# Optimization experiments

Hardware: AMD Instinct MI355X
Metric: run time of the kernel (lower is better)

The kernel has to match this reference:

```python
import jax, jax.numpy as jnp
import numpy as np

BS, SEQ, ML, DEPTH = 32, 50, 16, 4
NN = 2 ** DEPTH - 1          # 15 nodes per complete binary tree (heap layout)
VOCAB, EMB, ENC = 50000, 128, 128
GH = 32                      # bigru hidden per direction
NC = 100                     # num_concepts
LH = 128                     # LSTM hidden
LIN = 2 + 2 * GH + NC + 1    # 167 LSTM feature dim


def _gru_dir(x, Wx, Wh, bx, bh, reverse):
    # x: [B, T, I]; torch GRU gate order r,z,n
    B, H = x.shape[0], Wh.shape[1]
    xe = jnp.einsum('bti,gi->btg', x, Wx) + bx   # [B,T,3H]
    xs = jnp.swapaxes(xe, 0, 1)
    if reverse:
        xs = xs[::-1]
    def step(h, xt):
        gh = h @ Wh.T + bh
        r = jax.nn.sigmoid(xt[:, :H] + gh[:, :H])
        z = jax.nn.sigmoid(xt[:, H:2 * H] + gh[:, H:2 * H])
        n = jnp.tanh(xt[:, 2 * H:] + r * gh[:, 2 * H:])
        hn = (1.0 - z) * n + z * h
        return hn, hn
    _, hs = jax.lax.scan(step, jnp.zeros((B, H), x.dtype), xs)
    if reverse:
        hs = hs[::-1]
    return jnp.swapaxes(hs, 0, 1)


def _lstm(x, Wx, Wh, bx, bh):
    # x: [B, T, I]; torch LSTM gate order i,f,g,o
    B, H = x.shape[0], Wh.shape[1]
    xe = jnp.einsum('bti,gi->btg', x, Wx) + bx   # [B,T,4H]
    def step(carry, xt):
        h, c = carry
        g = xt + h @ Wh.T + bh
        i = jax.nn.sigmoid(g[:, :H])
        f = jax.nn.sigmoid(g[:, H:2 * H])
        gg = jnp.tanh(g[:, 2 * H:3 * H])
        o = jax.nn.sigmoid(g[:, 3 * H:])
        c = f * c + i * gg
        h = o * jnp.tanh(c)
        return (h, c), h
    h0 = (jnp.zeros((B, H), x.dtype), jnp.zeros((B, H), x.dtype))
    _, hs = jax.lax.scan(step, h0, jnp.swapaxes(xe, 0, 1))
    return jnp.swapaxes(hs, 0, 1)


def setup_inputs() -> dict:
    key = jax.random.key(0)
    ks = jax.random.split(key, 24)
    p = {}
    p['p_id'] = jax.random.randint(ks[0], (BS, SEQ), 0, 1000)
    p['c_id'] = jax.random.randint(ks[1], (BS, SEQ), 0, NC)
    p['ast_tokens'] = jax.random.randint(ks[2], (BS, SEQ, ML, NN), 0, VOCAB)
    p['target_c'] = jax.nn.one_hot(jax.random.randint(ks[3], (BS, SEQ), 0, NC + 1), NC + 1, dtype=jnp.float32)
    p['c_embed'] = jax.random.normal(ks[4], (BS, SEQ, NC + 1), jnp.float32)
    p['cur_result'] = jax.random.normal(ks[5], (BS, SEQ, 2), jnp.float32)
    p['result'] = (jax.random.uniform(ks[6], (BS * SEQ,)) < 0.5).astype(jnp.float32)
    p['emb'] = jax.random.normal(ks[7], (VOCAB, EMB), jnp.float32) * 0.02
    p['Wc_w'] = jax.random.normal(ks[8], (ENC, EMB), jnp.float32) / np.sqrt(EMB)
    p['Wc_b'] = jnp.zeros((ENC,), jnp.float32)
    p['gru_WxF'] = jax.random.normal(ks[9], (3 * GH, ENC), jnp.float32) / np.sqrt(ENC)
    p['gru_WhF'] = jax.random.normal(ks[10], (3 * GH, GH), jnp.float32) / np.sqrt(GH)
    p['gru_bxF'] = jnp.zeros((3 * GH,), jnp.float32)
    p['gru_bhF'] = jnp.zeros((3 * GH,), jnp.float32)
    p['gru_WxB'] = jax.random.normal(ks[11], (3 * GH, ENC), jnp.float32) / np.sqrt(ENC)
    p['gru_WhB'] = jax.random.normal(ks[12], (3 * GH, GH), jnp.float32) / np.sqrt(GH)
    p['gru_bxB'] = jnp.zeros((3 * GH,), jnp.float32)
    p['gru_bhB'] = jnp.zeros((3 * GH,), jnp.float32)
    p['lstm_Wx'] = jax.random.normal(ks[13], (4 * LH, LIN), jnp.float32) / np.sqrt(LIN)
    p['lstm_Wh'] = jax.random.normal(ks[14], (4 * LH, LH), jnp.float32) / np.sqrt(LH)
    p['lstm_bx'] = jnp.zeros((4 * LH,), jnp.float32)
    p['lstm_bh'] = jnp.zeros((4 * LH,), jnp.float32)
    p['pred_w'] = jax.random.normal(ks[15], (NC + 1, LH), jnp.float32) / np.sqrt(LH)
    p['pred_b'] = jnp.zeros((NC + 1,), jnp.float32)
    return p


def reference(p_id, c_id, ast_tokens, target_c, c_embed, cur_result, result,
              emb, Wc_w, Wc_b,
              gru_WxF, gru_WhF, gru_bxF, gru_bhF,
              gru_WxB, gru_WhB, gru_bxB, gru_bhB,
              lstm_Wx, lstm_Wh, lstm_bx, lstm_bh,
              pred_w, pred_b):
    # BatchTreeEncoder: per-node W_c(emb(tok)), subtree-sum via bottom-up heap, max over nodes
    e = emb[ast_tokens] @ Wc_w.T + Wc_b          # [BS,SEQ,ML,NN,ENC]
    s = e
    for lvl in range(DEPTH - 2, -1, -1):          # bottom-up over fixed tree levels
        par = np.arange(2 ** lvl - 1, 2 ** (lvl + 1) - 1)
        s = s.at[..., par, :].add(s[..., 2 * par + 1, :] + s[..., 2 * par + 2, :])
    tree_enc = jnp.max(s, axis=3)                 # [BS,SEQ,ML,ENC]
    x = tree_enc.reshape(BS * SEQ, ML, ENC)
    hf = _gru_dir(x, gru_WxF, gru_WhF, gru_bxF, gru_bhF, False)
    hb = _gru_dir(x, gru_WxB, gru_WhB, gru_bxB, gru_bhB, True)
    gout = jnp.concatenate([hf, hb], axis=-1)     # [BS*SEQ, ML, 64]
    code = jnp.max(gout, axis=1).reshape(BS, SEQ, 2 * GH)  # max_pool1d over time
    lin = jnp.concatenate([c_embed, code, cur_result], axis=-1)  # [BS,SEQ,LIN]
    lout = _lstm(lin, lstm_Wx, lstm_Wh, lstm_bx, lstm_bh)         # [BS,SEQ,LH]
    pred = lout.reshape(BS * SEQ, LH) @ pred_w.T + pred_b         # [BS*SEQ, NC+1]
    tc = target_c.reshape(BS * SEQ, NC + 1)
    p1 = jnp.sum(pred * tc, axis=-1)              # bmm(pred, target_c)
    ncon = jnp.sum(tc, axis=-1)
    m = (ncon > 0).astype(pred.dtype)
    fp = p1 / jnp.maximum(ncon, 1.0)
    bce = jnp.maximum(fp, 0.0) - fp * result + jnp.log1p(jnp.exp(-jnp.abs(fp)))
    loss = jnp.sum(bce * m) / jnp.maximum(jnp.sum(m), 1.0)
    return loss, jax.nn.sigmoid(fp) * m, result * m
```

## Files before the change

### kernel.cpp

```cpp
#include <hip/hip_runtime.h>
#include <hip/hip_bf16.h>
#include <math.h>

#define BS 32
#define SEQ 50
#define ML 16
#define NN 15
#define NTREE (BS*SEQ*ML)
#define NROW (BS*SEQ)
#define VOCAB 50000
#define EMB 128
#define ENC 128
#define GH 32
#define NC 100
#define LH 128
#define LIN_D 167

typedef float f32x4 __attribute__((ext_vector_type(4)));
typedef short s16x8 __attribute__((ext_vector_type(8)));
typedef unsigned int u32;
typedef u32 u32x4v __attribute__((ext_vector_type(4)));

#define LOG2E 1.4426950408889634f
__device__ __forceinline__ float fsig(float x) {
  return __builtin_amdgcn_rcpf(1.f + __builtin_amdgcn_exp2f(-LOG2E * x));
}
__device__ __forceinline__ float ftanh(float x) {
  return 2.f * __builtin_amdgcn_rcpf(
             1.f + __builtin_amdgcn_exp2f(-2.f * LOG2E * x)) - 1.f;
}
__device__ __forceinline__ u32 pkbf(float x, float y) {
  u32 a = __float_as_uint(x), b = __float_as_uint(y);
  a = (a + 0x7FFFu + ((a >> 16) & 1u)) >> 16;
  b = (b + 0x7FFFu + ((b >> 16) & 1u)) >> 16;
  return a | (b << 16);
}
__device__ __forceinline__ unsigned short f2bf(float x) {
  u32 a = __float_as_uint(x);
  return (unsigned short)((a + 0x7FFFu + ((a >> 16) & 1u)) >> 16);
}
#define MFMA __builtin_amdgcn_mfma_f32_16x16x32_bf16

__global__ __launch_bounds__(256) void gemm_mfma(
    const float* __restrict__ A, const u32* __restrict__ Bpk,
    const float* __restrict__ bias, void* __restrict__ Cout,
    int M, int N, int out_bf16) {
  int w = threadIdx.x >> 6, lane = threadIdx.x & 63;
  int R0 = blockIdx.x * 64 + w * 16;
  int r = R0 + (lane & 15);
  int rm = (r < M) ? r : (M - 1);
  const float* Ar = A + (size_t)rm * 128 + (lane >> 4) * 8;
  s16x8 a0, a1, a2, a3;
  {
#define LDA(AF, KT) { \
    float4 f0 = *(const float4*)(Ar + KT * 32); \
    float4 f1 = *(const float4*)(Ar + KT * 32 + 4); \
    u32x4v q = {pkbf(f0.x, f0.y), pkbf(f0.z, f0.w), \
                pkbf(f1.x, f1.y), pkbf(f1.z, f1.w)}; \
    AF = __builtin_bit_cast(s16x8, q); }
    LDA(a0, 0) LDA(a1, 1) LDA(a2, 2) LDA(a3, 3)
#undef LDA
  }
  const u32x4v* Bp = (const u32x4v*)Bpk;
  for (int c = 0; c < N; c += 64) {
    f32x4 acc0, acc1, acc2, acc3;
    {
      float b0 = bias ? bias[c + (lane & 15)]      : 0.f;
      float b1 = bias ? bias[c + 16 + (lane & 15)] : 0.f;
      float b2 = bias ? bias[c + 32 + (lane & 15)] : 0.f;
      float b3 = bias ? bias[c + 48 + (lane & 15)] : 0.f;
      acc0 = (f32x4){b0, b0, b0, b0}; acc1 = (f32x4){b1, b1, b1, b1};
      acc2 = (f32x4){b2, b2, b2, b2}; acc3 = (f32x4){b3, b3, b3, b3};
    }
    int fbase = (c >> 4) * 4;
#define DONT(ACC, NT) { \
    s16x8 bf0 = __builtin_bit_cast(s16x8, Bp[(size_t)(fbase + NT * 4 + 0) * 64 + lane]); \
    s16x8 bf1 = __builtin_bit_cast(s16x8, Bp[(size_t)(fbase + NT * 4 + 1) * 64 + lane]); \
    s16x8 bf2 = __builtin_bit_cast(s16x8, Bp[(size_t)(fbase + NT * 4 + 2) * 64 + lane]); \
    s16x8 bf3 = __builtin_bit_cast(s16x8, Bp[(size_t)(fbase + NT * 4 + 3) * 64 + lane]); \
    ACC = MFMA(a0, bf0, ACC, 0, 0, 0); ACC = MFMA(a1, bf1, ACC, 0, 0, 0); \
    ACC = MFMA(a2, bf2, ACC, 0, 0, 0); ACC = MFMA(a3, bf3, ACC, 0, 0, 0); }
    DONT(acc0, 0) DONT(acc1, 1) DONT(acc2, 2) DONT(acc3, 3)
#undef DONT
    int colb = c + (lane & 15);
    int rowb = R0 + (lane >> 4) * 4;
#define STNT(ACC, NT) \
    _Pragma("unroll") \
    for (int j = 0; j < 4; j++) { \
      int row = rowb + j; \
      if (row < M) { \
        if (out_bf16) ((unsigned short*)Cout)[(size_t)row * N + colb + NT * 16] = f2bf(ACC[j]); \
        else ((float*)Cout)[(size_t)row * N + colb + NT * 16] = ACC[j]; \
      } \
    }
    STNT(acc0, 0) STNT(acc1, 1) STNT(acc2, 2) STNT(acc3, 3)
#undef STNT
  }
}

__global__ __launch_bounds__(256) void k_tree_xe(
    const int* __restrict__ ast, const u32* __restrict__ Epb,
    const float* __restrict__ Wc_b, const u32* __restrict__ Bpk,
    const float* __restrict__ bias, float* __restrict__ Cout) {
  __shared__ int toks[64 * 15];
  int t = threadIdx.x, w = t >> 6, lane = t & 63;
  int R0 = blockIdx.x * 64;
  const int* ab = ast + (size_t)R0 * 15;
  #pragma unroll
  for (int i = t; i < 960; i += 256) toks[i] = ab[i];
  __syncthreads();
  int rl = w * 16 + (lane & 15);
  int q = lane >> 4;
  const u32x4v* Epg = (const u32x4v*)Epb;
  s16x8 afr0, afr1, afr2, afr3;
#define BUILD(AF, KT) { \
    u32x4v g[15]; \
    _Pragma("unroll") \
    for (int n = 0; n < 15; n++) \
      g[n] = Epg[(size_t)toks[rl * 15 + n] * 16 + KT * 4 + q]; \
    u32 outw[4]; \
    _Pragma("unroll") \
    for (int j = 0; j < 4; j++) { \
      float m2[2]; \
      _Pragma("unroll") \
      for (int hilo = 0; hilo < 2; hilo++) { \
        float e[15]; \
        _Pragma("unroll") \
        for (int n = 0; n < 15; n++) \
          e[n] = __uint_as_float(hilo ? (g[n][j] & 0xFFFF0000u) : (g[n][j] << 16)); \
        float b = Wc_b[KT * 32 + q * 8 + 2 * j + hilo]; \
        float s3 = e[3] + e[7] + e[8],  s4 = e[4] + e[9] + e[10]; \
        float s5 = e[5] + e[11] + e[12], s6 = e[6] + e[13] + e[14]; \
        float s1 = e[1] + s3 + s4, s2 = e[2] + s5 + s6; \
        float s0 = e[0] + s1 + s2; \
        float ml = fmaxf(fmaxf(fmaxf(e[7], e[8]), fmaxf(e[9], e[10])), \
                         fmaxf(fmaxf(e[11], e[12]), fmaxf(e[13], e[14]))) + b; \
        float mm = fmaxf(fmaxf(s3, s4), fmaxf(s5, s6)) + 3.f * b; \
        float mt = fmaxf(s1, s2) + 7.f * b; \
        m2[hilo] = fmaxf(fmaxf(ml, mm), fmaxf(mt, s0 + 15.f * b)); \
      } \
      outw[j] = pkbf(m2[0], m2[1]); \
    } \
    u32x4v qq = {outw[0], outw[1], outw[2], outw[3]}; \
    AF = __builtin_bit_cast(s16x8, qq); }
  BUILD(afr0, 0) BUILD(afr1, 1) BUILD(afr2, 2) BUILD(afr3, 3)
#undef BUILD
  const u32x4v* Bp = (const u32x4v*)Bpk;
  int R0w = R0 + w * 16;
  for (int c = 0; c < 192; c += 64) {
    f32x4 acc0, acc1, acc2, acc3;
// ... 31 lines not shown
    int row, int k) {
  if (k < 101) return ce[row * 101 + k];
  if (k < 165) return co[row * 64 + (k - 101)];
  if (k < 167) return cu[row * 2 + (k - 165)];
  return 0.f;
}

__global__ __launch_bounds__(256) void gemm_lin(
    const float* __restrict__ c_embed, const float* __restrict__ code,
    const float* __restrict__ cur, const u32* __restrict__ Bpk,
    const float* __restrict__ bias, float* __restrict__ Cout) {
  int w = threadIdx.x >> 6, lane = threadIdx.x & 63;
  int R0 = blockIdx.x * 64 + w * 16;
  int r = R0 + (lane & 15);
  s16x8 a[6];
  #pragma unroll
  for (int kt = 0; kt < 6; kt++) {
    int k0 = kt * 32 + (lane >> 4) * 8;
    float f[8];
    #pragma unroll
    for (int j = 0; j < 8; j++) f[j] = lin_at(c_embed, code, cur, r, k0 + j);
    u32x4v q = {pkbf(f[0], f[1]), pkbf(f[2], f[3]),
                pkbf(f[4], f[5]), pkbf(f[6], f[7])};
    a[kt] = __builtin_bit_cast(s16x8, q);
  }
  const u32x4v* Bp = (const u32x4v*)Bpk;
  for (int c = 0; c < 512; c += 64) {
    f32x4 acc[4];
    #pragma unroll
    for (int nt = 0; nt < 4; nt++) {
      float bv = bias[c + nt * 16 + (lane & 15)];
      acc[nt] = (f32x4){bv, bv, bv, bv};
    }
    int fbase = (c >> 4) * 6;
    #pragma unroll
    for (int nt = 0; nt < 4; nt++) {
      #pragma unroll
      for (int kt = 0; kt < 6; kt++) {
        s16x8 bf = __builtin_bit_cast(s16x8,
            Bp[(size_t)(fbase + nt * 6 + kt) * 64 + lane]);
        acc[nt] = MFMA(a[kt], bf, acc[nt], 0, 0, 0);
      }
    }
    int colb = c + (lane & 15);
    int rowb = R0 + (lane >> 4) * 4;
    #pragma unroll
    for (int nt = 0; nt < 4; nt++)
      #pragma unroll
      for (int j = 0; j < 4; j++)
        Cout[(size_t)(rowb + j) * 512 + colb + nt * 16] = acc[nt][j];
  }
}

__global__ __launch_bounds__(256) void k_prep(const float* __restrict__ WxF,
    const float* __restrict__ WxB, const float* __restrict__ bxF,
    const float* __restrict__ bxB, const float* __restrict__ lstm_Wx,
    const float* __restrict__ lstm_Wh, const float* __restrict__ Wc_w,
    const float* __restrict__ gru_WhF, const float* __restrict__ gru_WhB,
    float* __restrict__ ball, u32* __restrict__ Wcpk,
    u32* __restrict__ Wallpk, u32* __restrict__ Wxpk, u32* __restrict__ Wpk,
    u32* __restrict__ Wgpk) {
  int i = blockIdx.x * 256 + threadIdx.x;
  if (i < 96) ball[i] = bxF[i];
  else if (i < 192) ball[i] = bxB[i - 96];
  if (i < 8192) {
    int fg = i >> 8, l = (i >> 2) & 63, p = i & 3;
    int nt = fg >> 2, kt = fg & 3;
    int n = nt * 16 + (l & 15);
    int k = kt * 32 + (l >> 4) * 8 + 2 * p;
    Wcpk[i] = pkbf(Wc_w[n * 128 + k], Wc_w[n * 128 + k + 1]);
  }
  if (i < 12288) {
    int fg = i >> 8, l = (i >> 2) & 63, p = i & 3;
    int nt = fg >> 2, kt = fg & 3;
    int n = nt * 16 + (l & 15);
    int k = kt * 32 + (l >> 4) * 8 + 2 * p;
    float v0 = (n < 96) ? WxF[n * 128 + k]     : WxB[(n - 96) * 128 + k];
    float v1 = (n < 96) ? WxF[n * 128 + k + 1] : WxB[(n - 96) * 128 + k + 1];
    Wallpk[i] = pkbf(v0, v1);
  }
  if (i < 49152) {
    int fg = i >> 8, l = (i >> 2) & 63, p = i & 3;
    int nt = fg / 6, kt = fg % 6;
    int n = nt * 16 + (l & 15);
    int k = kt * 32 + (l >> 4) * 8 + 2 * p;
    float v0 = (k < LIN_D)     ? lstm_Wx[n * LIN_D + k]     : 0.f;
    float v1 = (k + 1 < LIN_D) ? lstm_Wx[n * LIN_D + k + 1] : 0.f;
    Wxpk[i] = pkbf(v0, v1);
  }
  if (i < 32768) {
    int fg = i >> 8, l = (i >> 2) & 63, p = i & 3;
    int w = fg >> 4, gt = (fg >> 2) & 3, kt = fg & 3;
    int n = 128 * gt + 16 * w + (l & 15);
    int k = 32 * kt + 8 * (l >> 4) + 2 * p;
    Wpk[i] = pkbf(lstm_Wh[n * 128 + k], lstm_Wh[n * 128 + k + 1]);
  }
  if (i < 3072) {
    int fg = i >> 8, l = (i >> 2) & 63, p = i & 3;
    int dir = fg / 6, nt = fg % 6;
    int n = nt * 16 + (l & 15);
    int k = (l >> 4) * 8 + 2 * p;
    const float* Wh = dir ? gru_WhB : gru_WhF;
    Wgpk[i] = pkbf(Wh[n * 32 + k], Wh[n * 32 + k + 1]);
  }
}

__global__ __launch_bounds__(256) void k_gru(const float* __restrict__ xe_all,
    const u32* __restrict__ Wgpk, const float* __restrict__ bhF,
    const float* __restrict__ bhB, float* __restrict__ code) {
  __shared__ float xls[32 * 192];
  __shared__ short hls[4][32];
  int t = threadIdx.x, w = t >> 6, lane = t & 63;
  int sq0 = blockIdx.x * 2;
  const float* xb = xe_all + (size_t)sq0 * 16 * 192;
  #pragma unroll 4
  for (int i = t; i < 32 * 192; i += 256) xls[i] = xb[i];
  int sql = w >> 1, dir = w & 1;
  int seq = sq0 + sql;
  const s16x8* BG = (const s16x8*)Wgpk + (size_t)dir * 6 * 64 + lane;
  s16x8 G0 = BG[0], G1 = BG[64], G2 = BG[128];
  s16x8 G3 = BG[192], G4 = BG[256], G5 = BG[320];
  const float* bh = dir ? bhB : bhF;
  float bh0 = 0, bh1 = 0, bh2 = 0, bh3 = 0, bh4 = 0, bh5 = 0;
  if (lane < 16) {
    bh0 = bh[lane];      bh1 = bh[16 + lane]; bh2 = bh[32 + lane];
    bh3 = bh[48 + lane]; bh4 = bh[64 + lane]; bh5 = bh[80 + lane];
  }
  float h0 = 0.f, h1 = 0.f, mx0 = -1e30f, mx1 = -1e30f;
  hls[w][lane & 31] = 0;
  __syncthreads();
  const s16x8 zz = {0, 0, 0, 0, 0, 0, 0, 0};
  const bool arow = (lane & 15) == 0;
  const int aoff = (lane >> 4) * 8;
  for (int s = 0; s < 16; s++) {
    int tt = dir ? (15 - s) : s;
    const float* xr = xls + (sql * 16 + tt) * 192 + dir * 96;
    s16x8 a = arow ? *(const s16x8*)&hls[w][aoff] : zz;
    f32x4 ac0 = {0,0,0,0}, ac1 = {0,0,0,0}, ac2 = {0,0,0,0};
    f32x4 ac3 = {0,0,0,0}, ac4 = {0,0,0,0}, ac5 = {0,0,0,0};
    float xn0 = 0.f, xn1 = 0.f;
    if (lane < 16) {
      ac0[0] = xr[lane] + bh0;      ac1[0] = xr[16 + lane] + bh1;
      ac2[0] = xr[32 + lane] + bh2; ac3[0] = xr[48 + lane] + bh3;
      ac4[0] = bh4;                 ac5[0] = bh5;
      xn0 = xr[64 + lane];          xn1 = xr[80 + lane];
    }
    ac0 = MFMA(a, G0, ac0, 0, 0, 0); ac1 = MFMA(a, G1, ac1, 0, 0, 0);
    ac2 = MFMA(a, G2, ac2, 0, 0, 0); ac3 = MFMA(a, G3, ac3, 0, 0, 0);
    ac4 = MFMA(a, G4, ac4, 0, 0, 0); ac5 = MFMA(a, G5, ac5, 0, 0, 0);
    if (lane < 16) {
      float r0 = fsig(ac0[0]), r1 = fsig(ac1[0]);
      float z0 = fsig(ac2[0]), z1 = fsig(ac3[0]);
      float n0 = ftanh(xn0 + r0 * ac4[0]);
      float n1 = ftanh(xn1 + r1 * ac5[0]);
      h0 = (1.f - z0) * n0 + z0 * h0;
      h1 = (1.f - z1) * n1 + z1 * h1;
      mx0 = fmaxf(mx0, h0); mx1 = fmaxf(mx1, h1);
      hls[w][lane]      = (short)f2bf(h0);
      hls[w][16 + lane] = (short)f2bf(h1);
    }
  }
  if (lane < 16) {
    code[(size_t)seq * 64 + dir * 32 + lane]      = mx0;
    code[(size_t)seq * 64 + dir * 32 + 16 + lane] = mx1;
  }
}

__global__ __launch_bounds__(512) void k_lstm(
    const float* __restrict__ xeL, const u32* __restrict__ Wpk,
    const float* __restrict__ bh, float* __restrict__ lout) {
  __shared__ float xl[SEQ * 512];
  __shared__ float hh[SEQ * 128];
  __shared__ s16x8 hl8[16];
  short* hls = (short*)hl8;
  int b = blockIdx.x, t = threadIdx.x;
  int w = t >> 6, lane = t & 63;
  const float* xrow = xeL + (size_t)b * SEQ * 512;
  #pragma unroll 5
  for (int i = t; i < SEQ * 512; i += 512) xl[i] = xrow[i];
  const s16x8* WB = (const s16x8*)Wpk + (size_t)w * 16 * 64 + lane;
  s16x8 B00 = WB[0*64],  B01 = WB[1*64],  B02 = WB[2*64],  B03 = WB[3*64];
  s16x8 B10 = WB[4*64],  B11 = WB[5*64],  B12 = WB[6*64],  B13 = WB[7*64];
  s16x8 B20 = WB[8*64],  B21 = WB[9*64],  B22 = WB[10*64], B23 = WB[11*64];
  s16x8 B30 = WB[12*64], B31 = WB[13*64], B32 = WB[14*64], B33 = WB[15*64];

  int u16 = 16 * w + lane;
  float bh0 = 0, bh1 = 0, bh2 = 0, bh3 = 0;
  if (lane < 16) {
    bh0 = bh[u16]; bh1 = bh[128 + u16]; bh2 = bh[256 + u16]; bh3 = bh[384 + u16];
  }
  float c = 0.f;
  if (t < 128) hls[t] = 0;
  __syncthreads();
  const s16x8 zz = {0, 0, 0, 0, 0, 0, 0, 0};
  const bool arow = (lane & 15) == 0;
  const int asel = lane >> 4;
  for (int step = 0; step < SEQ; step++) {
    s16x8 a0 = arow ? hl8[asel]      : zz;
    s16x8 a1 = arow ? hl8[4 + asel]  : zz;
    s16x8 a2 = arow ? hl8[8 + asel]  : zz;
    s16x8 a3 = arow ? hl8[12 + asel] : zz;
    f32x4 acc0 = {0, 0, 0, 0}, acc1 = {0, 0, 0, 0};
    f32x4 acc2 = {0, 0, 0, 0}, acc3 = {0, 0, 0, 0};
    if (lane < 16) {
      const float* xs = xl + step * 512;
      acc0[0] = xs[u16]       + bh0;
      acc1[0] = xs[128 + u16] + bh1;
      acc2[0] = xs[256 + u16] + bh2;
      acc3[0] = xs[384 + u16] + bh3;
    }
    acc0 = MFMA(a0, B00, acc0, 0, 0, 0); acc0 = MFMA(a1, B01, acc0, 0, 0, 0);
    acc0 = MFMA(a2, B02, acc0, 0, 0, 0); acc0 = MFMA(a3, B03, acc0, 0, 0, 0);
    acc1 = MFMA(a0, B10, acc1, 0, 0, 0); acc1 = MFMA(a1, B11, acc1, 0, 0, 0);
    acc1 = MFMA(a2, B12, acc1, 0, 0, 0); acc1 = MFMA(a3, B13, acc1, 0, 0, 0);
    acc2 = MFMA(a0, B20, acc2, 0, 0, 0); acc2 = MFMA(a1, B21, acc2, 0, 0, 0);
    acc2 = MFMA(a2, B22, acc2, 0, 0, 0); acc2 = MFMA(a3, B23, acc2, 0, 0, 0);
    acc3 = MFMA(a0, B30, acc3, 0, 0, 0); acc3 = MFMA(a1, B31, acc3, 0, 0, 0);
    acc3 = MFMA(a2, B32, acc3, 0, 0, 0); acc3 = MFMA(a3, B33, acc3, 0, 0, 0);
    if (lane < 16) {
      float iv = fsig(acc0[0]);
      float fv = fsig(acc1[0]);
      float gv = ftanh(acc2[0]);
      float ov = fsig(acc3[0]);
      c = fv * c + iv * gv;
      float h = ov * ftanh(c);
      hh[step * 128 + u16] = h;
      hls[u16] = (short)f2bf(h);
    }
    __syncthreads();
  }
  float* lo = lout + (size_t)b * SEQ * 128;
  #pragma unroll 4
  for (int i = t; i < SEQ * 128; i += 512) lo[i] = hh[i];
}

__global__ __launch_bounds__(128) void k_pred(const float* __restrict__ lout,
    const float* __restrict__ pred_w, const float* __restrict__ pred_b,
    const float* __restrict__ tc, const float* __restrict__ result,
    float* __restrict__ out, float* __restrict__ fpbuf, float* __restrict__ mbuf) {
  int row = blockIdx.x; int k = threadIdx.x;
  __shared__ float tcs[101];
  __shared__ float r1[128], r2[128], r3[128];
  if (k < 101) tcs[k] = tc[(size_t)row * 101 + k];
  __syncthreads();
  float nz = 0.f, ixs = 0.f, vs = 0.f;
  if (k < 101 && tcs[k] != 0.f) { nz = 1.f; ixs = (float)k; vs = tcs[k]; }
  r1[k] = nz; r2[k] = ixs; r3[k] = vs;
  __syncthreads();
  for (int st = 64; st > 0; st >>= 1) {
    if (k < st) { r1[k] += r1[k + st]; r2[k] += r2[k + st]; r3[k] += r3[k + st]; }
    __syncthreads();
  }
  float cnt = r1[0], idxf = r2[0], ncon = r3[0];
  __syncthreads();
  float fp, m;
  if (cnt == 1.f && ncon == 1.f) {
    int cls = (int)idxf;
    float v = lout[(size_t)row * 128 + k] * pred_w[cls * 128 + k];
    r1[k] = v;
    __syncthreads();
    for (int st = 64; st > 0; st >>= 1) {
      if (k < st) r1[k] += r1[k + st];
      __syncthreads();
    }
    fp = r1[0] + pred_b[cls];
    m = 1.f;
  } else {
    float lk = lout[(size_t)row * 128 + k];
    float acc = 0.f;
    for (int c = 0; c < 101; c++) acc += tcs[c] * pred_w[c * 128 + k];
    float v = acc * lk;
    float pb = (k < 101) ? tcs[k] * pred_b[k] : 0.f;
    r1[k] = v; r2[k] = pb;
    __syncthreads();
    for (int st = 64; st > 0; st >>= 1) {
      if (k < st) { r1[k] += r1[k + st]; r2[k] += r2[k + st]; }
      __syncthreads();
    }
    m = (ncon > 0.f) ? 1.f : 0.f;
    fp = (r1[0] + r2[0]) / fmaxf(ncon, 1.f);
  }
  if (k == 0) {
    fpbuf[row] = fp; mbuf[row] = m;
    out[1 + row] = m / (1.f + expf(-fp));
    out[1 + NROW + row] = result[row] * m;
  }
}

__global__ __launch_bounds__(256) void k_loss(const float* __restrict__ fpbuf,
    const float* __restrict__ mbuf, const float* __restrict__ result,
    float* __restrict__ out) {
  __shared__ float sb[256], sm[256];
  int k = threadIdx.x;
  float ab = 0.f, am = 0.f;
  for (int r = k; r < NROW; r += 256) {
    float fp = fpbuf[r], m = mbuf[r], res = result[r];
    float bce = fmaxf(fp, 0.f) - fp * res + log1pf(expf(-fabsf(fp)));
    ab += bce * m; am += m;
  }
  sb[k] = ab; sm[k] = am;
  __syncthreads();
  for (int st = 128; st > 0; st >>= 1) {
    if (k < st) { sb[k] += sb[k + st]; sm[k] += sm[k + st]; }
    __syncthreads();
  }
  if (k == 0) out[0] = sb[0] / fmaxf(sm[0], 1.f);
}

extern "C" void kernel_launch(void* const* d_in, const int* in_sizes, int n_in,
                              void* d_out, int out_size, void* d_ws, size_t ws_size,
                              hipStream_t stream) {
  (void)in_sizes; (void)n_in; (void)out_size; (void)ws_size;
  const int*   ast      = (const int*)  d_in[2];
  const float* target_c = (const float*)d_in[3];
  const float* c_embed  = (const float*)d_in[4];
  const float* cur_res  = (const float*)d_in[5];
  const float* result   = (const float*)d_in[6];
  const float* emb      = (const float*)d_in[7];
  const float* Wc_w     = (const float*)d_in[8];
  const float* Wc_b     = (const float*)d_in[9];
  const float* gru_WxF  = (const float*)d_in[10];
  const float* gru_WhF  = (const float*)d_in[11];
  const float* gru_bxF  = (const float*)d_in[12];
  const float* gru_bhF  = (const float*)d_in[13];
  const float* gru_WxB  = (const float*)d_in[14];
  const float* gru_WhB  = (const float*)d_in[15];
  const float* gru_bxB  = (const float*)d_in[16];
  const float* gru_bhB  = (const float*)d_in[17];
  const float* lstm_Wx  = (const float*)d_in[18];
  const float* lstm_Wh  = (const float*)d_in[19];
  const float* lstm_bx  = (const float*)d_in[20];
  const float* lstm_bh  = (const float*)d_in[21];
  const float* pred_w   = (const float*)d_in[22];
  const float* pred_b   = (const float*)d_in[23];
  float* out = (float*)d_out;

  float* W = (float*)d_ws;
  u32*   Epb    = (u32*)W;
  float* xe_all = W + 3200000;
  float* code   = W + 8115200;
  float* xeL    = W + 8217600;
  float* lout   = W + 9036800;
  float* fpbuf  = W + 9241600;
  float* mbuf   = W + 9243200;
  u32*   Wcpk   = (u32*)(W + 9244800);
  u32*   Wallpk = (u32*)(W + 9252992);
  u32*   Wxpk   = (u32*)(W + 9265280);
  u32*   Wpk    = (u32*)(W + 9314432);
  float* ball   = W + 9347200;
  u32*   Wgpk   = (u32*)(W + 9347392);

  k_prep<<<192, 256, 0, stream>>>(gru_WxF, gru_WxB, gru_bxF, gru_bxB, lstm_Wx,
                                  lstm_Wh, Wc_w, gru_WhF, gru_WhB,
                                  ball, Wcpk, Wallpk, Wxpk, Wpk, Wgpk);
  gemm_mfma<<<782, 256, 0, stream>>>(emb, Wcpk, nullptr, Epb, VOCAB, 128, 1);
  k_tree_xe<<<400, 256, 0, stream>>>(ast, Epb, Wc_b, Wallpk, ball, xe_all);
  k_gru<<<NROW / 2, 256, 0, stream>>>(xe_all, Wgpk, gru_bhF, gru_bhB, code);
  gemm_lin<<<25, 256, 0, stream>>>(c_embed, code, cur_res, Wxpk, lstm_bx, xeL);
  k_lstm<<<BS, 512, 0, stream>>>(xeL, Wpk, lstm_bh, lout);
  k_pred<<<NROW, 128, 0, stream>>>(lout, pred_w, pred_b, target_c, result,
                                   out, fpbuf, mbuf);
  k_loss<<<1, 256, 0, stream>>>(fpbuf, mbuf, result, out);
}
```

Baseline: 134.1 us.

## Fuse weight prep into embedding GEMM and prediction head into LSTM kernel

The separate weight-packing kernel is folded into the embedding-projection GEMM launch as extra blocks. The GEMM now packs Wc_w from fp32 directly in registers instead of reading a pre-packed buffer. The prediction/gather kernel is merged into the LSTM kernel, which reads hidden states from shared memory and reduces with wave shuffles. Together these remove two launches and the lout global round trip. In exchange, each GEMM block re-reads and re-converts the fp32 weights, and the 32-block LSTM kernel takes on the extra prediction work.

New measurement: 179.1 us. 1.34x slower.

```diff
diff --git a/kernel.cpp b/kernel.cpp
--- a/kernel.cpp
+++ b/kernel.cpp
@@ -41,15 +41,60 @@
 }
 #define MFMA __builtin_amdgcn_mfma_f32_16x16x32_bf16
 
-__global__ __launch_bounds__(256) void gemm_mfma(
-    const float* __restrict__ A, const u32* __restrict__ Bpk,
-    const float* __restrict__ bias, void* __restrict__ Cout,
-    int M, int N, int out_bf16) {
+__global__ __launch_bounds__(256) void k_ep_prep(
+    const float* __restrict__ emb, const float* __restrict__ Wc_w,
+    const float* __restrict__ WxF, const float* __restrict__ WxB,
+    const float* __restrict__ bxF, const float* __restrict__ bxB,
+    const float* __restrict__ lstm_Wx, const float* __restrict__ lstm_Wh,
+    const float* __restrict__ gru_WhF, const float* __restrict__ gru_WhB,
+    unsigned short* __restrict__ Epb, float* __restrict__ ball,
+    u32* __restrict__ Wallpk, u32* __restrict__ Wxpk,
+    u32* __restrict__ Wpk, u32* __restrict__ Wgpk) {
+  int bid = blockIdx.x;
+  if (bid >= 782) {
+    int i = (bid - 782) * 256 + threadIdx.x;
+    if (i < 96) ball[i] = bxF[i];
+    else if (i < 192) ball[i] = bxB[i - 96];
+    if (i < 12288) {
+      int fg = i >> 8, l = (i >> 2) & 63, p = i & 3;
+      int nt = fg >> 2, kt = fg & 3;
+      int n = nt * 16 + (l & 15);
+      int k = kt * 32 + (l >> 4) * 8 + 2 * p;
+      float v0 = (n < 96) ? WxF[n * 128 + k]     : WxB[(n - 96) * 128 + k];
+      float v1 = (n < 96) ? WxF[n * 128 + k + 1] : WxB[(n - 96) * 128 + k + 1];
+      Wallpk[i] = pkbf(v0, v1);
+    }
+    if (i < 49152) {
+      int fg = i >> 8, l = (i >> 2) & 63, p = i & 3;
+      int nt = fg / 6, kt = fg % 6;
+      int n = nt * 16 + (l & 15);
+      int k = kt * 32 + (l >> 4) * 8 + 2 * p;
+      float v0 = (k < LIN_D)     ? lstm_Wx[n * LIN_D + k]     : 0.f;
+      float v1 = (k + 1 < LIN_D) ? lstm_Wx[n * LIN_D + k + 1] : 0.f;
+      Wxpk[i] = pkbf(v0, v1);
+    }
+    if (i < 32768) {
+      int fg = i >> 8, l = (i >> 2) & 63, p = i & 3;
+      int w = fg >> 4, gt = (fg >> 2) & 3, kt = fg & 3;
+      int n = 128 * gt + 16 * w + (l & 15);
+      int k = 32 * kt + 8 * (l >> 4) + 2 * p;
+      Wpk[i] = pkbf(lstm_Wh[n * 128 + k], lstm_Wh[n * 128 + k + 1]);
+    }
+    if (i < 3072) {
+      int fg = i >> 8, l = (i >> 2) & 63, p = i & 3;
+      int dir = fg / 6, nt = fg % 6;
+      int n = nt * 16 + (l & 15);
+      int k = (l >> 4) * 8 + 2 * p;
+      const float* Wh = dir ? gru_WhB : gru_WhF;
+      Wgpk[i] = pkbf(Wh[n * 32 + k], Wh[n * 32 + k + 1]);
+    }
+    return;
+  }
   int w = threadIdx.x >> 6, lane = threadIdx.x & 63;
-  int R0 = blockIdx.x * 64 + w * 16;
+  int R0 = bid * 64 + w * 16;
   int r = R0 + (lane & 15);
-  int rm = (r < M) ? r : (M - 1);
-  const float* Ar = A + (size_t)rm * 128 + (lane >> 4) * 8;
+  int rm = (r < VOCAB) ? r : (VOCAB - 1);
+  const float* Ar = emb + (size_t)rm * 128 + (lane >> 4) * 8;
   s16x8 a0, a1, a2, a3;
   {
 #define LDA(AF, KT) { \
@@ -61,23 +106,22 @@
     LDA(a0, 0) LDA(a1, 1) LDA(a2, 2) LDA(a3, 3)
 #undef LDA
   }
-  const u32x4v* Bp = (const u32x4v*)Bpk;
-  for (int c = 0; c < N; c += 64) {
-    f32x4 acc0, acc1, acc2, acc3;
-    {
-      float b0 = bias ? bias[c + (lane & 15)]      : 0.f;
-      float b1 = bias ? bias[c + 16 + (lane & 15)] : 0.f;
-      float b2 = bias ? bias[c + 32 + (lane & 15)] : 0.f;
-      float b3 = bias ? bias[c + 48 + (lane & 15)] : 0.f;
-      acc0 = (f32x4){b0, b0, b0, b0}; acc1 = (f32x4){b1, b1, b1, b1};
-      acc2 = (f32x4){b2, b2, b2, b2}; acc3 = (f32x4){b3, b3, b3, b3};
-    }
+#define BLDB(BF, FG) { \
+    int nn_ = ((FG) >> 2) * 16 + (lane & 15); \
+    int kq_ = ((FG) & 3) * 32 + (lane >> 4) * 8; \
+    const float* wr = Wc_w + nn_ * 128 + kq_; \
+    float4 f0 = *(const float4*)wr; float4 f1 = *(const float4*)(wr + 4); \
+    u32x4v q = {pkbf(f0.x, f0.y), pkbf(f0.z, f0.w), \
+                pkbf(f1.x, f1.y), pkbf(f1.z, f1.w)}; \
+    BF = __builtin_bit_cast(s16x8, q); }
+  for (int c = 0; c < 128; c += 64) {
+    f32x4 acc0 = {0,0,0,0}, acc1 = {0,0,0,0};
+    f32x4 acc2 = {0,0,0,0}, acc3 = {0,0,0,0};
     int fbase = (c >> 4) * 4;
 #define DONT(ACC, NT) { \
-    s16x8 bf0 = __builtin_bit_cast(s16x8, Bp[(size_t)(fbase + NT * 4 + 0) * 64 + lane]); \
-    s16x8 bf1 = __builtin_bit_cast(s16x8, Bp[(size_t)(fbase + NT * 4 + 1) * 64 + lane]); \
-    s16x8 bf2 = __builtin_bit_cast(s16x8, Bp[(size_t)(fbase + NT * 4 + 2) * 64 + lane]); \
-    s16x8 bf3 = __builtin_bit_cast(s16x8, Bp[(size_t)(fbase + NT * 4 + 3) * 64 + lane]); \
+    s16x8 bf0, bf1, bf2, bf3; \
+    BLDB(bf0, fbase + NT * 4 + 0) BLDB(bf1, fbase + NT * 4 + 1) \
+    BLDB(bf2, fbase + NT * 4 + 2) BLDB(bf3, fbase + NT * 4 + 3) \
     ACC = MFMA(a0, bf0, ACC, 0, 0, 0); ACC = MFMA(a1, bf1, ACC, 0, 0, 0); \
     ACC = MFMA(a2, bf2, ACC, 0, 0, 0); ACC = MFMA(a3, bf3, ACC, 0, 0, 0); }
     DONT(acc0, 0) DONT(acc1, 1) DONT(acc2, 2) DONT(acc3, 3)
@@ -88,14 +132,13 @@
     _Pragma("unroll") \
     for (int j = 0; j < 4; j++) { \
       int row = rowb + j; \
-      if (row < M) { \
-        if (out_bf16) ((unsigned short*)Cout)[(size_t)row * N + colb + NT * 16] = f2bf(ACC[j]); \
-        else ((float*)Cout)[(size_t)row * N + colb + NT * 16] = ACC[j]; \
-      } \
+      if (row < VOCAB) \
+        Epb[(size_t)row * 128 + colb + NT * 16] = f2bf(ACC[j]); \
     }
     STNT(acc0, 0) STNT(acc1, 1) STNT(acc2, 2) STNT(acc3, 3)
 #undef STNT
   }
+#undef BLDB
 }
 
 __global__ __launch_bounds__(256) void k_tree_xe(
@@ -233,59 +276,6 @@
   }
 }
 
-__global__ __launch_bounds__(256) void k_prep(const float* __restrict__ WxF,
-    const float* __restrict__ WxB, const float* __restrict__ bxF,
-    const float* __restrict__ bxB, const float* __restrict__ lstm_Wx,
-    const float* __restrict__ lstm_Wh, const float* __restrict__ Wc_w,
-    const float* __restrict__ gru_WhF, const float* __restrict__ gru_WhB,
-    float* __restrict__ ball, u32* __restrict__ Wcpk,
-    u32* __restrict__ Wallpk, u32* __restrict__ Wxpk, u32* __restrict__ Wpk,
-    u32* __restrict__ Wgpk) {
-  int i = blockIdx.x * 256 + threadIdx.x;
-  if (i < 96) ball[i] = bxF[i];
-  else if (i < 192) ball[i] = bxB[i - 96];
-  if (i < 8192) {
-    int fg = i >> 8, l = (i >> 2) & 63, p = i & 3;
-    int nt = fg >> 2, kt = fg & 3;
-    int n = nt * 16 + (l & 15);
-    int k = kt * 32 + (l >> 4) * 8 + 2 * p;
-    Wcpk[i] = pkbf(Wc_w[n * 128 + k], Wc_w[n * 128 + k + 1]);
-  }
-  if (i < 12288) {
-    int fg = i >> 8, l = (i >> 2) & 63, p = i & 3;
-    int nt = fg >> 2, kt = fg & 3;
-    int n = nt * 16 + (l & 15);
-    int k = kt * 32 + (l >> 4) * 8 + 2 * p;
-    float v0 = (n < 96) ? WxF[n * 128 + k]     : WxB[(n - 96) * 128 + k];
-    float v1 = (n < 96) ? WxF[n * 128 + k + 1] : WxB[(n - 96) * 128 + k + 1];
-    Wallpk[i] = pkbf(v0, v1);
-  }
-  if (i < 49152) {
-    int fg = i >> 8, l = (i >> 2) & 63, p = i & 3;
-    int nt = fg / 6, kt = fg % 6;
-    int n = nt * 16 + (l & 15);
-    int k = kt * 32 + (l >> 4) * 8 + 2 * p;
-    float v0 = (k < LIN_D)     ? lstm_Wx[n * LIN_D + k]     : 0.f;
-    float v1 = (k + 1 < LIN_D) ? lstm_Wx[n * LIN_D + k + 1] : 0.f;
-    Wxpk[i] = pkbf(v0, v1);
-  }
-  if (i < 32768) {
-    int fg = i >> 8, l = (i >> 2) & 63, p = i & 3;
-    int w = fg >> 4, gt = (fg >> 2) & 3, kt = fg & 3;
-    int n = 128 * gt + 16 * w + (l & 15);
-    int k = 32 * kt + 8 * (l >> 4) + 2 * p;
-    Wpk[i] = pkbf(lstm_Wh[n * 128 + k], lstm_Wh[n * 128 + k + 1]);
-  }
-  if (i < 3072) {
-    int fg = i >> 8, l = (i >> 2) & 63, p = i & 3;
-    int dir = fg / 6, nt = fg % 6;
-    int n = nt * 16 + (l & 15);
-    int k = (l >> 4) * 8 + 2 * p;
-    const float* Wh = dir ? gru_WhB : gru_WhF;
-    Wgpk[i] = pkbf(Wh[n * 32 + k], Wh[n * 32 + k + 1]);
-  }
-}
-
 __global__ __launch_bounds__(256) void k_gru(const float* __restrict__ xe_all,
     const u32* __restrict__ Wgpk, const float* __restrict__ bhF,
     const float* __restrict__ bhB, float* __restrict__ code) {
@@ -347,12 +337,16 @@
   }
 }
 
-__global__ __launch_bounds__(512) void k_lstm(
+__global__ __launch_bounds__(512) void k_lstm_pred(
     const float* __restrict__ xeL, const u32* __restrict__ Wpk,
-    const float* __restrict__ bh, float* __restrict__ lout) {
+    const float* __restrict__ bh, const float* __restrict__ pred_w,
+    const float* __restrict__ pred_b, const float* __restrict__ tc,
+    const float* __restrict__ result, float* __restrict__ out,
+    float* __restrict__ fpbuf, float* __restrict__ mbuf) {
   __shared__ float xl[SEQ * 512];
   __shared__ float hh[SEQ * 128];
   __shared__ s16x8 hl8[16];
+  __shared__ float tcl[8][104];
   short* hls = (short*)hl8;
   int b = blockIdx.x, t = threadIdx.x;
   int w = t >> 6, lane = t & 63;
@@ -410,61 +404,55 @@
     }
     __syncthreads();
   }
-  float* lo = lout + (size_t)b * SEQ * 128;
-  #pragma unroll 4
-  for (int i = t; i < SEQ * 128; i += 512) lo[i] = hh[i];
-}
-
-__global__ __launch_bounds__(128) void k_pred(const float* __restrict__ lout,
-    const float* __restrict__ pred_w, const float* __restrict__ pred_b,
-    const float* __restrict__ tc, const float* __restrict__ result,
-    float* __restrict__ out, float* __restrict__ fpbuf, float* __restrict__ mbuf) {
-  int row = blockIdx.x; int k = threadIdx.x;
-  __shared__ float tcs[101];
-  __shared__ float r1[128], r2[128], r3[128];
-  if (k < 101) tcs[k] = tc[(size_t)row * 101 + k];
-  __syncthreads();
-  float nz = 0.f, ixs = 0.f, vs = 0.f;
-  if (k < 101 && tcs[k] != 0.f) { nz = 1.f; ixs = (float)k; vs = tcs[k]; }
-  r1[k] = nz; r2[k] = ixs; r3[k] = vs;
-  __syncthreads();
-  for (int st = 64; st > 0; st >>= 1) {
-    if (k < st) { r1[k] += r1[k + st]; r2[k] += r2[k + st]; r3[k] += r3[k + st]; }
-    __syncthreads();
-  }
-  float cnt = r1[0], idxf = r2[0], ncon = r3[0];
-  __syncthreads();
-  float fp, m;
-  if (cnt == 1.f && ncon == 1.f) {
-    int cls = (int)idxf;
-    float v = lout[(size_t)row * 128 + k] * pred_w[cls * 128 + k];
-    r1[k] = v;
-    __syncthreads();
-    for (int st = 64; st > 0; st >>= 1) {
-      if (k < st) r1[k] += r1[k + st];
-      __syncthreads();
-    }
-    fp = r1[0] + pred_b[cls];
-    m = 1.f;
-  } else {
-    float lk = lout[(size_t)row * 128 + k];
-    float acc = 0.f;
-    for (int c = 0; c < 101; c++) acc += tcs[c] * pred_w[c * 128 + k];
-    float v = acc * lk;
-    float pb = (k < 101) ? tcs[k] * pred_b[k] : 0.f;
-    r1[k] = v; r2[k] = pb;
-    __syncthreads();
-    for (int st = 64; st > 0; st >>= 1) {
-      if (k < st) { r1[k] += r1[k + st]; r2[k] += r2[k + st]; }
-      __syncthreads();
-    }
-    m = (ncon > 0.f) ? 1.f : 0.f;
-    fp = (r1[0] + r2[0]) / fmaxf(ncon, 1.f);
-  }
-  if (k == 0) {
-    fpbuf[row] = fp; mbuf[row] = m;
-    out[1 + row] = m / (1.f + expf(-fp));
-    out[1 + NROW + row] = result[row] * m;
+  for (int tr = w; tr < SEQ; tr += 8) {
+    int row = b * SEQ + tr;
+    const float* tcr = tc + (size_t)row * 101;
+    float tc0 = tcr[lane];
+    float tc1 = (lane < 37) ? tcr[64 + lane] : 0.f;
+    tcl[w][lane] = tc0;
+    if (lane < 37) tcl[w][64 + lane] = tc1;
+    float nz = ((tc0 != 0.f) ? 1.f : 0.f) + ((tc1 != 0.f) ? 1.f : 0.f);
+    float ixs = ((tc0 != 0.f) ? (float)lane : 0.f) +
+                ((tc1 != 0.f) ? (float)(64 + lane) : 0.f);
+    float vs = tc0 + tc1;
+    #pragma unroll
+    for (int mskk = 32; mskk; mskk >>= 1) {
+      nz  += __shfl_xor(nz, mskk);
+      ixs += __shfl_xor(ixs, mskk);
+      vs  += __shfl_xor(vs, mskk);
+    }
+    float fp, mval;
+    if (nz == 1.f && vs == 1.f) {
+      int cls = (int)ixs;
+      const float* pw = pred_w + cls * 128;
+      float p = hh[tr * 128 + lane] * pw[lane]
+              + hh[tr * 128 + 64 + lane] * pw[64 + lane];
+      #pragma unroll
+      for (int mskk = 32; mskk; mskk >>= 1) p += __shfl_xor(p, mskk);
+      fp = p + pred_b[cls];
+      mval = 1.f;
+    } else {
+      float v = 0.f;
+      #pragma unroll
+      for (int kk = 0; kk < 2; kk++) {
+        int k = lane + kk * 64;
+        float acc = 0.f;
+        for (int cc = 0; cc < 101; cc++) acc += tcl[w][cc] * pred_w[cc * 128 + k];
+        v += acc * hh[tr * 128 + k];
+      }
+      float pb = tc0 * pred_b[lane];
+      if (lane < 37) pb += tc1 * pred_b[64 + lane];
+      float tot = v + pb;
+      #pragma unroll
+      for (int mskk = 32; mskk; mskk >>= 1) tot += __shfl_xor(tot, mskk);
+      mval = (vs > 0.f) ? 1.f : 0.f;
+      fp = tot / fmaxf(vs, 1.f);
+    }
+    if (lane == 0) {
+      fpbuf[row] = fp; mbuf[row] = mval;
+      out[1 + row] = mval / (1.f + expf(-fp));
+      out[1 + NROW + row] = result[row] * mval;
+    }
   }
 }
 
@@ -521,25 +509,22 @@
   float* xe_all = W + 3200000;
   float* code   = W + 8115200;
   float* xeL    = W + 8217600;
-  float* lout   = W + 9036800;
-  float* fpbuf  = W + 9241600;
-  float* mbuf   = W + 9243200;
-  u32*   Wcpk   = (u32*)(W + 9244800);
-  u32*   Wallpk = (u32*)(W + 9252992);
-  u32*   Wxpk   = (u32*)(W + 9265280);
-  u32*   Wpk    = (u32*)(W + 9314432);
-  float* ball   = W + 9347200;
-  u32*   Wgpk   = (u32*)(W + 9347392);
-
-  k_prep<<<192, 256, 0, stream>>>(gru_WxF, gru_WxB, gru_bxF, gru_bxB, lstm_Wx,
-                                  lstm_Wh, Wc_w, gru_WhF, gru_WhB,
-                                  ball, Wcpk, Wallpk, Wxpk, Wpk, Wgpk);
-  gemm_mfma<<<782, 256, 0, stream>>>(emb, Wcpk, nullptr, Epb, VOCAB, 128, 1);
+  float* fpbuf  = W + 9036800;
+  float* mbuf   = W + 9038400;
+  u32*   Wallpk = (u32*)(W + 9040000);
+  u32*   Wxpk   = (u32*)(W + 9052288);
+  u32*   Wpk    = (u32*)(W + 9101440);
+  float* ball   = W + 9134208;
+  u32*   Wgpk   = (u32*)(W + 9134400);
+
+  k_ep_prep<<<974, 256, 0, stream>>>(emb, Wc_w, gru_WxF, gru_WxB, gru_bxF,
+                                     gru_bxB, lstm_Wx, lstm_Wh, gru_WhF,
+                                     gru_WhB, (unsigned short*)Epb, ball,
+                                     Wallpk, Wxpk, Wpk, Wgpk);
   k_tree_xe<<<400, 256, 0, stream>>>(ast, Epb, Wc_b, Wallpk, ball, xe_all);
   k_gru<<<NROW / 2, 256, 0, stream>>>(xe_all, Wgpk, gru_bhF, gru_bhB, code);
   gemm_lin<<<25, 256, 0, stream>>>(c_embed, code, cur_res, Wxpk, lstm_bx, xeL);
-  k_lstm<<<BS, 512, 0, stream>>>(xeL, Wpk, lstm_bh, lout);
-  k_pred<<<NROW, 128, 0, stream>>>(lout, pred_w, pred_b, target_c, result,
-                                   out, fpbuf, mbuf);
+  k_lstm_pred<<<BS, 512, 0, stream>>>(xeL, Wpk, lstm_bh, pred_w, pred_b,
+                                      target_c, result, out, fpbuf, mbuf);
   k_loss<<<1, 256, 0, stream>>>(fpbuf, mbuf, result, out);
 }
```

## Fuse weight prep into embedding GEMM and split LSTM MFMA accumulation chains

Applied to the files above, without the earlier changes.

Merges the weight-packing prep kernel and the vocab embedding projection GEMM into a single launch. The GEMM blocks now read and pack the Wc weights from fp32 directly instead of reading a pre-packed buffer, and the remaining prep work runs in extra trailing blocks. This removes one launch and the dependency between them. Separately, the LSTM recurrent step splits each 4-deep MFMA chain into two independent 2-deep chains that are summed afterwards, shortening the serial dependency per step. The cost is redundant fp32 weight loads and bf16 packing inside every GEMM block.

After: 153.5 us. +14.5%, slower.

```diff
diff --git a/kernel.cpp b/kernel.cpp
--- a/kernel.cpp
+++ b/kernel.cpp
@@ -41,15 +41,60 @@
 }
 #define MFMA __builtin_amdgcn_mfma_f32_16x16x32_bf16
 
-__global__ __launch_bounds__(256) void gemm_mfma(
-    const float* __restrict__ A, const u32* __restrict__ Bpk,
-    const float* __restrict__ bias, void* __restrict__ Cout,
-    int M, int N, int out_bf16) {
+__global__ __launch_bounds__(256) void k_ep_prep(
+    const float* __restrict__ emb, const float* __restrict__ Wc_w,
+    const float* __restrict__ WxF, const float* __restrict__ WxB,
+    const float* __restrict__ bxF, const float* __restrict__ bxB,
+    const float* __restrict__ lstm_Wx, const float* __restrict__ lstm_Wh,
+    const float* __restrict__ gru_WhF, const float* __restrict__ gru_WhB,
+    unsigned short* __restrict__ Epb, float* __restrict__ ball,
+    u32* __restrict__ Wallpk, u32* __restrict__ Wxpk,
+    u32* __restrict__ Wpk, u32* __restrict__ Wgpk) {
+  int bid = blockIdx.x;
+  if (bid >= 782) {
+    int i = (bid - 782) * 256 + threadIdx.x;
+    if (i < 96) ball[i] = bxF[i];
+    else if (i < 192) ball[i] = bxB[i - 96];
+    if (i < 12288) {
+      int fg = i >> 8, l = (i >> 2) & 63, p = i & 3;
+      int nt = fg >> 2, kt = fg & 3;
+      int n = nt * 16 + (l & 15);
+      int k = kt * 32 + (l >> 4) * 8 + 2 * p;
+      float v0 = (n < 96) ? WxF[n * 128 + k]     : WxB[(n - 96) * 128 + k];
+      float v1 = (n < 96) ? WxF[n * 128 + k + 1] : WxB[(n - 96) * 128 + k + 1];
+      Wallpk[i] = pkbf(v0, v1);
+    }
+    if (i < 49152) {
+      int fg = i >> 8, l = (i >> 2) & 63, p = i & 3;
+      int nt = fg / 6, kt = fg % 6;
+      int n = nt * 16 + (l & 15);
+      int k = kt * 32 + (l >> 4) * 8 + 2 * p;
+      float v0 = (k < LIN_D)     ? lstm_Wx[n * LIN_D + k]     : 0.f;
+      float v1 = (k + 1 < LIN_D) ? lstm_Wx[n * LIN_D + k + 1] : 0.f;
+      Wxpk[i] = pkbf(v0, v1);
+    }
+    if (i < 32768) {
+      int fg = i >> 8, l = (i >> 2) & 63, p = i & 3;
+      int w = fg >> 4, gt = (fg >> 2) & 3, kt = fg & 3;
+      int n = 128 * gt + 16 * w + (l & 15);
+      int k = 32 * kt + 8 * (l >> 4) + 2 * p;
+      Wpk[i] = pkbf(lstm_Wh[n * 128 + k], lstm_Wh[n * 128 + k + 1]);
+    }
+    if (i < 3072) {
+      int fg = i >> 8, l = (i >> 2) & 63, p = i & 3;
+      int dir = fg / 6, nt = fg % 6;
+      int n = nt * 16 + (l & 15);
+      int k = (l >> 4) * 8 + 2 * p;
+      const float* Wh = dir ? gru_WhB : gru_WhF;
+      Wgpk[i] = pkbf(Wh[n * 32 + k], Wh[n * 32 + k + 1]);
+    }
+    return;
+  }
   int w = threadIdx.x >> 6, lane = threadIdx.x & 63;
-  int R0 = blockIdx.x * 64 + w * 16;
+  int R0 = bid * 64 + w * 16;
   int r = R0 + (lane & 15);
-  int rm = (r < M) ? r : (M - 1);
-  const float* Ar = A + (size_t)rm * 128 + (lane >> 4) * 8;
+  int rm = (r < VOCAB) ? r : (VOCAB - 1);
+  const float* Ar = emb + (size_t)rm * 128 + (lane >> 4) * 8;
   s16x8 a0, a1, a2, a3;
   {
 #define LDA(AF, KT) { \
@@ -61,23 +106,22 @@
     LDA(a0, 0) LDA(a1, 1) LDA(a2, 2) LDA(a3, 3)
 #undef LDA
   }
-  const u32x4v* Bp = (const u32x4v*)Bpk;
-  for (int c = 0; c < N; c += 64) {
-    f32x4 acc0, acc1, acc2, acc3;
-    {
-      float b0 = bias ? bias[c + (lane & 15)]      : 0.f;
-      float b1 = bias ? bias[c + 16 + (lane & 15)] : 0.f;
-      float b2 = bias ? bias[c + 32 + (lane & 15)] : 0.f;
-      float b3 = bias ? bias[c + 48 + (lane & 15)] : 0.f;
-      acc0 = (f32x4){b0, b0, b0, b0}; acc1 = (f32x4){b1, b1, b1, b1};
-      acc2 = (f32x4){b2, b2, b2, b2}; acc3 = (f32x4){b3, b3, b3, b3};
-    }
+#define BLDB(BF, FG) { \
+    int nn_ = ((FG) >> 2) * 16 + (lane & 15); \
+    int kq_ = ((FG) & 3) * 32 + (lane >> 4) * 8; \
+    const float* wr = Wc_w + nn_ * 128 + kq_; \
+    float4 f0 = *(const float4*)wr; float4 f1 = *(const float4*)(wr + 4); \
+    u32x4v q = {pkbf(f0.x, f0.y), pkbf(f0.z, f0.w), \
+                pkbf(f1.x, f1.y), pkbf(f1.z, f1.w)}; \
+    BF = __builtin_bit_cast(s16x8, q); }
+  for (int c = 0; c < 128; c += 64) {
+    f32x4 acc0 = {0,0,0,0}, acc1 = {0,0,0,0};
+    f32x4 acc2 = {0,0,0,0}, acc3 = {0,0,0,0};
     int fbase = (c >> 4) * 4;
 #define DONT(ACC, NT) { \
-    s16x8 bf0 = __builtin_bit_cast(s16x8, Bp[(size_t)(fbase + NT * 4 + 0) * 64 + lane]); \
-    s16x8 bf1 = __builtin_bit_cast(s16x8, Bp[(size_t)(fbase + NT * 4 + 1) * 64 + lane]); \
-    s16x8 bf2 = __builtin_bit_cast(s16x8, Bp[(size_t)(fbase + NT * 4 + 2) * 64 + lane]); \
-    s16x8 bf3 = __builtin_bit_cast(s16x8, Bp[(size_t)(fbase + NT * 4 + 3) * 64 + lane]); \
+    s16x8 bf0, bf1, bf2, bf3; \
+    BLDB(bf0, fbase + NT * 4 + 0) BLDB(bf1, fbase + NT * 4 + 1) \
+    BLDB(bf2, fbase + NT * 4 + 2) BLDB(bf3, fbase + NT * 4 + 3) \
     ACC = MFMA(a0, bf0, ACC, 0, 0, 0); ACC = MFMA(a1, bf1, ACC, 0, 0, 0); \
     ACC = MFMA(a2, bf2, ACC, 0, 0, 0); ACC = MFMA(a3, bf3, ACC, 0, 0, 0); }
     DONT(acc0, 0) DONT(acc1, 1) DONT(acc2, 2) DONT(acc3, 3)
@@ -88,14 +132,13 @@
     _Pragma("unroll") \
     for (int j = 0; j < 4; j++) { \
       int row = rowb + j; \
-      if (row < M) { \
-        if (out_bf16) ((unsigned short*)Cout)[(size_t)row * N + colb + NT * 16] = f2bf(ACC[j]); \
-        else ((float*)Cout)[(size_t)row * N + colb + NT * 16] = ACC[j]; \
-      } \
+      if (row < VOCAB) \
+        Epb[(size_t)row * 128 + colb + NT * 16] = f2bf(ACC[j]); \
     }
     STNT(acc0, 0) STNT(acc1, 1) STNT(acc2, 2) STNT(acc3, 3)
 #undef STNT
   }
+#undef BLDB
 }
 
 __global__ __launch_bounds__(256) void k_tree_xe(
@@ -233,59 +276,6 @@
   }
 }
 
-__global__ __launch_bounds__(256) void k_prep(const float* __restrict__ WxF,
-    const float* __restrict__ WxB, const float* __restrict__ bxF,
-    const float* __restrict__ bxB, const float* __restrict__ lstm_Wx,
-    const float* __restrict__ lstm_Wh, const float* __restrict__ Wc_w,
-    const float* __restrict__ gru_WhF, const float* __restrict__ gru_WhB,
-    float* __restrict__ ball, u32* __restrict__ Wcpk,
-    u32* __restrict__ Wallpk, u32* __restrict__ Wxpk, u32* __restrict__ Wpk,
-    u32* __restrict__ Wgpk) {
-  int i = blockIdx.x * 256 + threadIdx.x;
-  if (i < 96) ball[i] = bxF[i];
-  else if (i < 192) ball[i] = bxB[i - 96];
-  if (i < 8192) {
-    int fg = i >> 8, l = (i >> 2) & 63, p = i & 3;
-    int nt = fg >> 2, kt = fg & 3;
-    int n = nt * 16 + (l & 15);
-    int k = kt * 32 + (l >> 4) * 8 + 2 * p;
-    Wcpk[i] = pkbf(Wc_w[n * 128 + k], Wc_w[n * 128 + k + 1]);
-  }
-  if (i < 12288) {
-    int fg = i >> 8, l = (i >> 2) & 63, p = i & 3;
-    int nt = fg >> 2, kt = fg & 3;
-    int n = nt * 16 + (l & 15);
-    int k = kt * 32 + (l >> 4) * 8 + 2 * p;
-    float v0 = (n < 96) ? WxF[n * 128 + k]     : WxB[(n - 96) * 128 + k];
-    float v1 = (n < 96) ? WxF[n * 128 + k + 1] : WxB[(n - 96) * 128 + k + 1];
-    Wallpk[i] = pkbf(v0, v1);
-  }
-  if (i < 49152) {
-    int fg = i >> 8, l = (i >> 2) & 63, p = i & 3;
-    int nt = fg / 6, kt = fg % 6;
-    int n = nt * 16 + (l & 15);
-    int k = kt * 32 + (l >> 4) * 8 + 2 * p;
-    float v0 = (k < LIN_D)     ? lstm_Wx[n * LIN_D + k]     : 0.f;
-    float v1 = (k + 1 < LIN_D) ? lstm_Wx[n * LIN_D + k + 1] : 0.f;
-    Wxpk[i] = pkbf(v0, v1);
-  }
-  if (i < 32768) {
-    int fg = i >> 8, l = (i >> 2) & 63, p = i & 3;
-    int w = fg >> 4, gt = (fg >> 2) & 3, kt = fg & 3;
-    int n = 128 * gt + 16 * w + (l & 15);
-    int k = 32 * kt + 8 * (l >> 4) + 2 * p;
-    Wpk[i] = pkbf(lstm_Wh[n * 128 + k], lstm_Wh[n * 128 + k + 1]);
-  }
-  if (i < 3072) {
-    int fg = i >> 8, l = (i >> 2) & 63, p = i & 3;
-    int dir = fg / 6, nt = fg % 6;
-    int n = nt * 16 + (l & 15);
-    int k = (l >> 4) * 8 + 2 * p;
-    const float* Wh = dir ? gru_WhB : gru_WhF;
-    Wgpk[i] = pkbf(Wh[n * 32 + k], Wh[n * 32 + k + 1]);
-  }
-}
-
 __global__ __launch_bounds__(256) void k_gru(const float* __restrict__ xe_all,
     const u32* __restrict__ Wgpk, const float* __restrict__ bhF,
     const float* __restrict__ bhB, float* __restrict__ code) {
@@ -374,6 +364,7 @@
   if (t < 128) hls[t] = 0;
   __syncthreads();
   const s16x8 zz = {0, 0, 0, 0, 0, 0, 0, 0};
+  const f32x4 zf = {0.f, 0.f, 0.f, 0.f};
   const bool arow = (lane & 15) == 0;
   const int asel = lane >> 4;
   for (int step = 0; step < SEQ; step++) {
@@ -381,8 +372,8 @@
     s16x8 a1 = arow ? hl8[4 + asel]  : zz;
     s16x8 a2 = arow ? hl8[8 + asel]  : zz;
     s16x8 a3 = arow ? hl8[12 + asel] : zz;
-    f32x4 acc0 = {0, 0, 0, 0}, acc1 = {0, 0, 0, 0};
-    f32x4 acc2 = {0, 0, 0, 0}, acc3 = {0, 0, 0, 0};
+    f32x4 acc0 = zf, acc1 = zf, acc2 = zf, acc3 = zf;
+    f32x4 t0 = zf, t1 = zf, t2 = zf, t3 = zf;
     if (lane < 16) {
       const float* xs = xl + step * 512;
       acc0[0] = xs[u16]       + bh0;
@@ -391,18 +382,18 @@
       acc3[0] = xs[384 + u16] + bh3;
     }
     acc0 = MFMA(a0, B00, acc0, 0, 0, 0); acc0 = MFMA(a1, B01, acc0, 0, 0, 0);
-    acc0 = MFMA(a2, B02, acc0, 0, 0, 0); acc0 = MFMA(a3, B03, acc0, 0, 0, 0);
+    t0   = MFMA(a2, B02, t0,   0, 0, 0); t0   = MFMA(a3, B03, t0,   0, 0, 0);
     acc1 = MFMA(a0, B10, acc1, 0, 0, 0); acc1 = MFMA(a1, B11, acc1, 0, 0, 0);
-    acc1 = MFMA(a2, B12, acc1, 0, 0, 0); acc1 = MFMA(a3, B13, acc1, 0, 0, 0);
+    t1   = MFMA(a2, B12, t1,   0, 0, 0); t1   = MFMA(a3, B13, t1,   0, 0, 0);
     acc2 = MFMA(a0, B20, acc2, 0, 0, 0); acc2 = MFMA(a1, B21, acc2, 0, 0, 0);
-    acc2 = MFMA(a2, B22, acc2, 0, 0, 0); acc2 = MFMA(a3, B23, acc2, 0, 0, 0);
+    t2   = MFMA(a2, B22, t2,   0, 0, 0); t2   = MFMA(a3, B23, t2,   0, 0, 0);
     acc3 = MFMA(a0, B30, acc3, 0, 0, 0); acc3 = MFMA(a1, B31, acc3, 0, 0, 0);
-    acc3 = MFMA(a2, B32, acc3, 0, 0, 0); acc3 = MFMA(a3, B33, acc3, 0, 0, 0);
+    t3   = MFMA(a2, B32, t3,   0, 0, 0); t3   = MFMA(a3, B33, t3,   0, 0, 0);
     if (lane < 16) {
-      float iv = fsig(acc0[0]);
-      float fv = fsig(acc1[0]);
-      float gv = ftanh(acc2[0]);
-      float ov = fsig(acc3[0]);
+      float iv = fsig(acc0[0] + t0[0]);
+      float fv = fsig(acc1[0] + t1[0]);
+      float gv = ftanh(acc2[0] + t2[0]);
+      float ov = fsig(acc3[0] + t3[0]);
       c = fv * c + iv * gv;
       float h = ov * ftanh(c);
       hh[step * 128 + u16] = h;
@@ -524,17 +515,16 @@
   float* lout   = W + 9036800;
   float* fpbuf  = W + 9241600;
   float* mbuf   = W + 9243200;
-  u32*   Wcpk   = (u32*)(W + 9244800);
-  u32*   Wallpk = (u32*)(W + 9252992);
-  u32*   Wxpk   = (u32*)(W + 9265280);
-  u32*   Wpk    = (u32*)(W + 9314432);
-  float* ball   = W + 9347200;
-  u32*   Wgpk   = (u32*)(W + 9347392);
-
-  k_prep<<<192, 256, 0, stream>>>(gru_WxF, gru_WxB, gru_bxF, gru_bxB, lstm_Wx,
-                                  lstm_Wh, Wc_w, gru_WhF, gru_WhB,
-                                  ball, Wcpk, Wallpk, Wxpk, Wpk, Wgpk);
-  gemm_mfma<<<782, 256, 0, stream>>>(emb, Wcpk, nullptr, Epb, VOCAB, 128, 1);
+  u32*   Wallpk = (u32*)(W + 9244800);
+  u32*   Wxpk   = (u32*)(W + 9257088);
+  u32*   Wpk    = (u32*)(W + 9306240);
+  float* ball   = W + 9339008;
+  u32*   Wgpk   = (u32*)(W + 9339200);
+
+  k_ep_prep<<<974, 256, 0, stream>>>(emb, Wc_w, gru_WxF, gru_WxB, gru_bxF,
+                                     gru_bxB, lstm_Wx, lstm_Wh, gru_WhF,
+                                     gru_WhB, (unsigned short*)Epb, ball,
+                                     Wallpk, Wxpk, Wpk, Wgpk);
   k_tree_xe<<<400, 256, 0, stream>>>(ast, Epb, Wc_b, Wallpk, ball, xe_all);
   k_gru<<<NROW / 2, 256, 0, stream>>>(xe_all, Wgpk, gru_bhF, gru_bhB, code);
   gemm_lin<<<25, 256, 0, stream>>>(c_embed, code, cur_res, Wxpk, lstm_bx, xeL);
```
